# Kernel tuning notes

Hardware: AMD Instinct MI355X
Metric: run time of the kernel (lower is better)

The kernel has to match this reference:

```python
import jax, jax.numpy as jnp
import numpy as np

H = 512  # hidden_dim

def setup_inputs() -> dict:
    key = jax.random.key(0)
    k1, k2, k3, k4, k5 = jax.random.split(key, 5)
    B, S = 32, 2048
    hidden = jax.random.normal(k1, (B, 2 * H), dtype=jnp.float32)
    encoder_outputs = jax.random.normal(k2, (B, S, 2 * H), dtype=jnp.float32)
    # nn.Linear(4H, H): weight [H, 4H], bias [H]
    W = jax.random.normal(k3, (H, 4 * H), dtype=jnp.float32) / np.sqrt(4 * H)
    b = jnp.zeros((H,), dtype=jnp.float32)
    v = jax.random.normal(k4, (H,), dtype=jnp.float32) / np.sqrt(H)
    return {"hidden": hidden, "encoder_outputs": encoder_outputs, "W": W, "b": b, "v": v}

def reference(hidden, encoder_outputs, W, b, v):
    B, S, _ = encoder_outputs.shape
    # concat repeated decoder hidden with encoder outputs: [B, S, 4H]
    hidden_rep = jnp.broadcast_to(hidden[:, None, :], (B, S, hidden.shape[-1]))
    cat = jnp.concatenate([hidden_rep, encoder_outputs], axis=-1)
    energy = jnp.tanh(jnp.einsum('bsf,hf->bsh', cat, W) + b)  # [B, S, H]
    scores = jnp.einsum('bsh,h->bs', energy, v)               # [B, S]
    attn = jax.nn.softmax(scores, axis=1)                     # softmax over seq
    context = jnp.einsum('bsd,bs->bd', encoder_outputs, attn) # [B, 2H]
    return context
```

## Files before the change

kernel.cpp:

```cpp
#include <hip/hip_runtime.h>


typedef __fp16   half2v __attribute__((ext_vector_type(2)));
typedef _Float16 half8  __attribute__((ext_vector_type(8)));
typedef __attribute__((ext_vector_type(4)))  float f4;
typedef __attribute__((ext_vector_type(16))) float f16v;
typedef __attribute__((ext_vector_type(4)))  unsigned int uint4v;

__device__ __forceinline__ void gload_lds16(const void* g, void* l) {
    __builtin_amdgcn_global_load_lds(
        (const __attribute__((address_space(1))) unsigned int*)g,
        (__attribute__((address_space(3))) unsigned int*)l, 16, 0, 0);
}
__device__ __forceinline__ unsigned int bc2(half2v h) {
    return __builtin_bit_cast(unsigned int, h);
}

__global__ __launch_bounds__(256) void prep_kernel(
    const float* __restrict__ hidden, const float* __restrict__ W,
    const float* __restrict__ bias, float* __restrict__ u,
    unsigned short* __restrict__ w2) {
    __shared__ float hid_s[1024];
    if (blockIdx.x < 256) {
        int g = blockIdx.x * 256 + threadIdx.x;
        int kk = g >> 11, id = g & 2047;
        int ntg = id >> 7, kh = (id >> 6) & 1, l = id & 63;
        int h = (ntg << 5) + (l & 31);
        int kg = 1024 + (kk << 5) + (kh << 4) + ((l >> 5) << 3);
        const float* src = W + (size_t)h * 2048 + kg;
        f4 x0 = *(const f4*)src;
        f4 x1 = *(const f4*)(src + 4);
        half8 vh;
        #pragma unroll
        for (int j = 0; j < 4; ++j) vh[j] = (_Float16)x0[j];
        #pragma unroll
        for (int j = 0; j < 4; ++j) vh[4 + j] = (_Float16)x1[j];
        ((half8*)w2)[g] = vh;
    } else {
        const int t = threadIdx.x;
        const int blk = (int)blockIdx.x - 256;
        const int b = blk >> 3, hg = blk & 7;
        ((f4*)hid_s)[t] = ((const f4*)(hidden + ((size_t)b << 10)))[t];
        __syncthreads();
        const int w = t >> 6, lane = t & 63;
        const f4* hid4 = (const f4*)hid_s;
        #pragma unroll 2
        for (int i = 0; i < 16; ++i) {
            int h = (hg << 6) + (w << 4) + i;
            const f4* wr = (const f4*)(W + (size_t)h * 2048);
            float p = 0.f;
            #pragma unroll
            for (int i2 = 0; i2 < 4; ++i2) {
                f4 w4 = wr[lane + (i2 << 6)];
                f4 h4 = hid4[lane + (i2 << 6)];
                p += w4[0]*h4[0] + w4[1]*h4[1] + w4[2]*h4[2] + w4[3]*h4[3];
            }
            #pragma unroll
            for (int off = 1; off < 64; off <<= 1) p += __shfl_xor(p, off);
            if (lane == 0) u[((size_t)b << 9) + h] = bias[h] + p;
        }
    }
}

__global__ __launch_bounds__(256, 3) void score_kernel(
    const float* __restrict__ enc, const unsigned short* __restrict__ w2,
    const float* __restrict__ u, const float* __restrict__ v,
    float* __restrict__ scores_part) {
    __shared__ short Ahi[2048], Alo[2048];
    __shared__ short Bs[8192];
    __shared__ float u_s[256], v_s[256];
    __shared__ float partial[4][64];

    const int tid  = threadIdx.x;
    const int wl   = tid >> 6, lane = tid & 63;
    const int col  = lane & 31;
    const int sblk = blockIdx.x >> 1, hh = blockIdx.x & 1;
    const int row0 = sblk * 64;
    const int b    = row0 >> 11;
    const float* encB = enc + (size_t)row0 * 1024;

    u_s[tid] = u[(b << 9) + (hh << 8) + tid];
    v_s[tid] = v[(hh << 8) + tid];

    f16v acc[2][2];
    #pragma unroll
    for (int mt = 0; mt < 2; ++mt)
        #pragma unroll
        for (int nt = 0; nt < 2; ++nt)
            #pragma unroll
            for (int r = 0; r < 16; ++r) acc[mt][nt][r] = 0.f;

    const int s_mt = tid >> 7, s_kh = (tid >> 6) & 1, s_l = tid & 63;
    const int s_row = (s_mt << 5) + (s_l & 31);
    const int s_kb  = (s_kh << 4) + ((s_l >> 5) << 3);
    const float* aSrc = encB + (size_t)s_row * 1024 + s_kb;

    const half8* Ah8 = (const half8*)Ahi;
    const half8* Al8 = (const half8*)Alo;
    const half8* Bh8 = (const half8*)Bs;

    for (int kk = 0; kk < 32; ++kk) {
        f4 x0 = *(const f4*)(aSrc + (kk << 5));
        f4 x1 = *(const f4*)(aSrc + (kk << 5) + 4);
        __syncthreads();
        {
            half2v h01 = __builtin_amdgcn_cvt_pkrtz(x0[0], x0[1]);
            half2v h23 = __builtin_amdgcn_cvt_pkrtz(x0[2], x0[3]);
            half2v h45 = __builtin_amdgcn_cvt_pkrtz(x1[0], x1[1]);
            half2v h67 = __builtin_amdgcn_cvt_pkrtz(x1[2], x1[3]);
            half2v l01 = __builtin_amdgcn_cvt_pkrtz(x0[0] - (float)h01[0], x0[1] - (float)h01[1]);
            half2v l23 = __builtin_amdgcn_cvt_pkrtz(x0[2] - (float)h23[0], x0[3] - (float)h23[1]);
            half2v l45 = __builtin_amdgcn_cvt_pkrtz(x1[0] - (float)h45[0], x1[1] - (float)h45[1]);
            half2v l67 = __builtin_amdgcn_cvt_pkrtz(x1[2] - (float)h67[0], x1[3] - (float)h67[1]);
            uint4v hp = {bc2(h01), bc2(h23), bc2(h45), bc2(h67)};
            uint4v lp = {bc2(l01), bc2(l23), bc2(l45), bc2(l67)};
            ((uint4v*)Ahi)[tid] = hp;
            ((uint4v*)Alo)[tid] = lp;
        }
        {
            const char* bsrc = (const char*)w2 + (size_t)kk * 32768 + (hh << 14)
                               + (wl << 12) + lane * 16;
            char* bdst = (char*)Bs + (wl << 12);
            #pragma unroll
            for (int i = 0; i < 4; ++i)
                gload_lds16(bsrc + (i << 10), bdst + (i << 10));
        }
        __syncthreads();
        #pragma unroll
        for (int kh = 0; kh < 2; ++kh) {
            half8 ah0 = Ah8[(kh << 6) + lane];
            half8 ah1 = Ah8[128 + (kh << 6) + lane];
            half8 al0 = Al8[(kh << 6) + lane];
            half8 al1 = Al8[128 + (kh << 6) + lane];
            #pragma unroll
            for (int nt = 0; nt < 2; ++nt) {
                int ntl = (wl << 1) + nt;
                half8 b8 = Bh8[((ntl << 1) + kh) * 64 + lane];
                acc[0][nt] = __builtin_amdgcn_mfma_f32_32x32x16_f16(ah0, b8, acc[0][nt], 0, 0, 0);
                acc[0][nt] = __builtin_amdgcn_mfma_f32_32x32x16_f16(al0, b8, acc[0][nt], 0, 0, 0);
                acc[1][nt] = __builtin_amdgcn_mfma_f32_32x32x16_f16(ah1, b8, acc[1][nt], 0, 0, 0);
                acc[1][nt] = __builtin_amdgcn_mfma_f32_32x32x16_f16(al1, b8, acc[1][nt], 0, 0, 0);
            }
        }
    }
    const int rhalf = (lane >> 5) << 2;
    #pragma unroll
    for (int mt = 0; mt < 2; ++mt) {
        #pragma unroll
        for (int reg = 0; reg < 16; ++reg) {
            float ssum = 0.f;
            #pragma unroll
            for (int nt = 0; nt < 2; ++nt) {
                int hl = (((wl << 1) + nt) << 5) + col;
                float x = u_s[hl] + acc[mt][nt][reg];
                float t = __expf(2.f * x);
                float th = 1.f - 2.f / (t + 1.f);
                ssum += v_s[hl] * th;
            }
            ssum += __shfl_xor(ssum, 1);
            ssum += __shfl_xor(ssum, 2);
            ssum += __shfl_xor(ssum, 4);
            ssum += __shfl_xor(ssum, 8);
            ssum += __shfl_xor(ssum, 16);
            if (col == 0)
                partial[wl][(mt << 5) + (reg & 3) + ((reg >> 2) << 3) + rhalf] = ssum;
        }
    }
    __syncthreads();
    if (tid < 64) {
        float s = partial[0][tid] + partial[1][tid] + partial[2][tid] + partial[3][tid];
        scores_part[(hh << 16) + row0 + tid] = s;
    }
}

__global__ __launch_bounds__(256) void ctx_partial_kernel(
    const float* __restrict__ enc, const float* __restrict__ scores_part,
    float* __restrict__ partials) {
    __shared__ float p_s[2048];
    __shared__ float wredm[4], wreds[4];
    const int t = threadIdx.x;
    const int b = blockIdx.x >> 5, sc = blockIdx.x & 31;
    const int wid = t >> 6, lane = t & 63;
    const float* s0 = scores_part + ((size_t)b << 11);
    const float* s1 = s0 + 65536;

    float vals[8];
    float mx = -1e30f;
    #pragma unroll
    for (int i = 0; i < 8; ++i) {
        int idx = t + (i << 8);
        vals[i] = s0[idx] + s1[idx];
        mx = fmaxf(mx, vals[i]);
    }
    #pragma unroll
    for (int off = 1; off < 64; off <<= 1) mx = fmaxf(mx, __shfl_xor(mx, off));
    if (lane == 0) wredm[wid] = mx;
    __syncthreads();
    mx = fmaxf(fmaxf(wredm[0], wredm[1]), fmaxf(wredm[2], wredm[3]));

    float lsum = 0.f;
    #pragma unroll
    for (int i = 0; i < 8; ++i) {
        float e = __expf(vals[i] - mx);
        p_s[t + (i << 8)] = e;
        lsum += e;
    }
    #pragma unroll
    for (int off = 1; off < 64; off <<= 1) lsum += __shfl_xor(lsum, off);
    if (lane == 0) wreds[wid] = lsum;
    __syncthreads();
    const float inv = 1.f / (wreds[0] + wreds[1] + wreds[2] + wreds[3]);

    f4 a0 = (f4){0.f, 0.f, 0.f, 0.f};
    f4 a1 = (f4){0.f, 0.f, 0.f, 0.f};
    f4 a2 = (f4){0.f, 0.f, 0.f, 0.f};
    f4 a3 = (f4){0.f, 0.f, 0.f, 0.f};
    const f4* erow = ((const f4*)(enc + ((size_t)b * 2048 + (sc << 6)) * 1024)) + t;
    #pragma unroll 4
    for (int i = 0; i < 64; i += 4) {
        a0 += p_s[(sc << 6) + i]     * erow[(size_t)i << 8];
        a1 += p_s[(sc << 6) + i + 1] * erow[((size_t)(i + 1)) << 8];
        a2 += p_s[(sc << 6) + i + 2] * erow[((size_t)(i + 2)) << 8];
        a3 += p_s[(sc << 6) + i + 3] * erow[((size_t)(i + 3)) << 8];
    }
    f4 a = ((a0 + a1) + (a2 + a3)) * inv;
    f4* dst = (f4*)(partials + (((size_t)(sc << 5) + b) << 10));
    dst[t] = a;
}

__global__ __launch_bounds__(256) void ctx_reduce_kernel(
    const float* __restrict__ partials, float* __restrict__ out) {
    int i = blockIdx.x * 256 + threadIdx.x;
    float s = 0.f;
    #pragma unroll
    for (int sc = 0; sc < 32; ++sc) s += partials[sc * 32768 + i];
    out[i] = s;
}

extern "C" void kernel_launch(void* const* d_in, const int* in_sizes, int n_in,
                              void* d_out, int out_size, void* d_ws, size_t ws_size,
                              hipStream_t stream) {
    const float* hidden = (const float*)d_in[0];
    const float* enc    = (const float*)d_in[1];
    const float* W      = (const float*)d_in[2];
    const float* bias   = (const float*)d_in[3];
    const float* v      = (const float*)d_in[4];
    float* out = (float*)d_out;
    char* ws = (char*)d_ws;

    float* u            = (float*)(ws);
    float* scores_part  = (float*)(ws + 65536);
    float* partials     = (float*)(ws + 589824);
    unsigned short* w2  = (unsigned short*)(ws + 4784128);

    prep_kernel<<<512, 256, 0, stream>>>(hidden, W, bias, u, w2);
    score_kernel<<<2048, 256, 0, stream>>>(enc, w2, u, v, scores_part);
    ctx_partial_kernel<<<1024, 256, 0, stream>>>(enc, scores_part, partials);
    ctx_reduce_kernel<<<128, 256, 0, stream>>>(partials, out);
}
```

Before: 518.9 us.

## Remap score blocks across XCDs and fuse context partial and reduce kernels

The score kernel now permutes block indices so that consecutive logical tiles land on different XCDs, with the aim of spreading L2 traffic. The separate context-partial and context-reduce kernels are merged into one kernel. In it, each 512-thread block owns a batch and a 128-float column slice, loops over all 2048 sequence rows, and reduces inside the block through LDS. This removes the partials buffer round-trip and one launch. The cost is only 256 blocks for the memory-bound pass over the encoder outputs, which may leave the GPU underused.

```diff
diff --git a/kernel.cpp b/kernel.cpp
--- a/kernel.cpp
+++ b/kernel.cpp
@@ -74,7 +74,9 @@
     const int tid  = threadIdx.x;
     const int wl   = tid >> 6, lane = tid & 63;
     const int col  = lane & 31;
-    const int sblk = blockIdx.x >> 1, hh = blockIdx.x & 1;
+    const int bid  = blockIdx.x;
+    const int lid  = ((bid & 7) << 8) + (bid >> 3);
+    const int sblk = lid >> 1, hh = lid & 1;
     const int row0 = sblk * 64;
     const int b    = row0 >> 11;
     const float* encB = enc + (size_t)row0 * 1024;
@@ -173,22 +175,23 @@
     }
 }
 
-__global__ __launch_bounds__(256) void ctx_partial_kernel(
+__global__ __launch_bounds__(512) void ctx_kernel(
     const float* __restrict__ enc, const float* __restrict__ scores_part,
-    float* __restrict__ partials) {
+    float* __restrict__ out) {
     __shared__ float p_s[2048];
-    __shared__ float wredm[4], wreds[4];
+    __shared__ float wredm[8], wreds[8];
+    __shared__ f4 red[16][32];
     const int t = threadIdx.x;
-    const int b = blockIdx.x >> 5, sc = blockIdx.x & 31;
+    const int b = blockIdx.x >> 3, dg = blockIdx.x & 7;
     const int wid = t >> 6, lane = t & 63;
     const float* s0 = scores_part + ((size_t)b << 11);
     const float* s1 = s0 + 65536;
 
-    float vals[8];
+    float vals[4];
     float mx = -1e30f;
     #pragma unroll
-    for (int i = 0; i < 8; ++i) {
-        int idx = t + (i << 8);
+    for (int i = 0; i < 4; ++i) {
+        int idx = t + (i << 9);
         vals[i] = s0[idx] + s1[idx];
         mx = fmaxf(mx, vals[i]);
     }
@@ -196,45 +199,51 @@
     for (int off = 1; off < 64; off <<= 1) mx = fmaxf(mx, __shfl_xor(mx, off));
     if (lane == 0) wredm[wid] = mx;
     __syncthreads();
-    mx = fmaxf(fmaxf(wredm[0], wredm[1]), fmaxf(wredm[2], wredm[3]));
-
-    float lsum = 0.f;
-    #pragma unroll
-    for (int i = 0; i < 8; ++i) {
-        float e = __expf(vals[i] - mx);
-        p_s[t + (i << 8)] = e;
-        lsum += e;
+    #pragma unroll
+    for (int i = 0; i < 8; ++i) mx = fmaxf(mx, wredm[i]);
+
+    float e[4], lsum = 0.f;
+    #pragma unroll
+    for (int i = 0; i < 4; ++i) {
+        e[i] = __expf(vals[i] - mx);
+        lsum += e[i];
     }
     #pragma unroll
     for (int off = 1; off < 64; off <<= 1) lsum += __shfl_xor(lsum, off);
     if (lane == 0) wreds[wid] = lsum;
     __syncthreads();
-    const float inv = 1.f / (wreds[0] + wreds[1] + wreds[2] + wreds[3]);
-
-    f4 a0 = (f4){0.f, 0.f, 0.f, 0.f};
-    f4 a1 = (f4){0.f, 0.f, 0.f, 0.f};
-    f4 a2 = (f4){0.f, 0.f, 0.f, 0.f};
-    f4 a3 = (f4){0.f, 0.f, 0.f, 0.f};
-    const f4* erow = ((const f4*)(enc + ((size_t)b * 2048 + (sc << 6)) * 1024)) + t;
-    #pragma unroll 4
-    for (int i = 0; i < 64; i += 4) {
-        a0 += p_s[(sc << 6) + i]     * erow[(size_t)i << 8];
-        a1 += p_s[(sc << 6) + i + 1] * erow[((size_t)(i + 1)) << 8];
-        a2 += p_s[(sc << 6) + i + 2] * erow[((size_t)(i + 2)) << 8];
-        a3 += p_s[(sc << 6) + i + 3] * erow[((size_t)(i + 3)) << 8];
-    }
-    f4 a = ((a0 + a1) + (a2 + a3)) * inv;
-    f4* dst = (f4*)(partials + (((size_t)(sc << 5) + b) << 10));
-    dst[t] = a;
-}
-
-__global__ __launch_bounds__(256) void ctx_reduce_kernel(
-    const float* __restrict__ partials, float* __restrict__ out) {
-    int i = blockIdx.x * 256 + threadIdx.x;
-    float s = 0.f;
-    #pragma unroll
-    for (int sc = 0; sc < 32; ++sc) s += partials[sc * 32768 + i];
-    out[i] = s;
+    float tot = 0.f;
+    #pragma unroll
+    for (int i = 0; i < 8; ++i) tot += wreds[i];
+    const float inv = 1.f / tot;
+    #pragma unroll
+    for (int i = 0; i < 4; ++i) p_s[t + (i << 9)] = e[i] * inv;
+    __syncthreads();
+
+    const int col = t & 31, rg = t >> 5;
+    const f4* e4 = (const f4*)enc;
+    const size_t base = (((size_t)b << 11) << 8) + (dg << 5) + col;
+    f4 a0 = (f4){0.f,0.f,0.f,0.f}, a1 = (f4){0.f,0.f,0.f,0.f};
+    f4 a2 = (f4){0.f,0.f,0.f,0.f}, a3 = (f4){0.f,0.f,0.f,0.f};
+    #pragma unroll 2
+    for (int i = 0; i < 128; i += 4) {
+        int r0 = ((i + 0) << 4) + rg;
+        int r1 = ((i + 1) << 4) + rg;
+        int r2 = ((i + 2) << 4) + rg;
+        int r3 = ((i + 3) << 4) + rg;
+        a0 += p_s[r0] * e4[base + ((size_t)r0 << 8)];
+        a1 += p_s[r1] * e4[base + ((size_t)r1 << 8)];
+        a2 += p_s[r2] * e4[base + ((size_t)r2 << 8)];
+        a3 += p_s[r3] * e4[base + ((size_t)r3 << 8)];
+    }
+    red[rg][col] = (a0 + a1) + (a2 + a3);
+    __syncthreads();
+    if (t < 32) {
+        f4 s = red[0][t];
+        #pragma unroll
+        for (int g = 1; g < 16; ++g) s += red[g][t];
+        ((f4*)out)[(b << 8) + (dg << 5) + t] = s;
+    }
 }
 
 extern "C" void kernel_launch(void* const* d_in, const int* in_sizes, int n_in,
@@ -250,11 +259,9 @@
 
     float* u            = (float*)(ws);
     float* scores_part  = (float*)(ws + 65536);
-    float* partials     = (float*)(ws + 589824);
-    unsigned short* w2  = (unsigned short*)(ws + 4784128);
+    unsigned short* w2  = (unsigned short*)(ws + 589824);
 
     prep_kernel<<<512, 256, 0, stream>>>(hidden, W, bias, u, w2);
     score_kernel<<<2048, 256, 0, stream>>>(enc, w2, u, v, scores_part);
-    ctx_partial_kernel<<<1024, 256, 0, stream>>>(enc, scores_part, partials);
-    ctx_reduce_kernel<<<128, 256, 0, stream>>>(partials, out);
-}
+    ctx_kernel<<<256, 512, 0, stream>>>(enc, scores_part, out);
+}
```

New measurement: 517.4 us. Within noise of the previous version (-0.3%).
